# Kernel tuning notes

Hardware: AMD Instinct MI355X
Metric: run time of the kernel (lower is better)

The kernel has to match this reference:

```python
import jax, jax.numpy as jnp
import numpy as np

EMBED_DIM = 1024
NUM_HEADS = 16
HEAD_DIM = EMBED_DIM // NUM_HEADS
B, S = 2, 2048


def setup_inputs() -> dict:
    key = jax.random.key(0)
    ks = jax.random.split(key, 12)
    sd = 1.0 / np.sqrt(EMBED_DIM)
    def lin(kw, kb):
        W = jax.random.uniform(kw, (EMBED_DIM, EMBED_DIM), jnp.float32, -sd, sd)
        b = jax.random.uniform(kb, (EMBED_DIM,), jnp.float32, -sd, sd)
        return W, b
    Wq, bq = lin(ks[0], ks[1])
    Wk, bk = lin(ks[2], ks[3])
    Wv, bv = lin(ks[4], ks[5])
    Wo, bo = lin(ks[6], ks[7])
    q = jax.random.normal(ks[8], (B, S, EMBED_DIM), jnp.float32)
    k = jax.random.normal(ks[9], (B, S, EMBED_DIM), jnp.float32)
    v = jax.random.normal(ks[10], (B, S, EMBED_DIM), jnp.float32)
    # broadcastable causal mask: True = keep (mask==0 positions get -inf)
    attn_mask = jnp.tril(jnp.ones((S, S), jnp.bool_))[None, None]
    return {"q": q, "k": k, "v": v,
            "Wq": Wq, "bq": bq, "Wk": Wk, "bk": bk,
            "Wv": Wv, "bv": bv, "Wo": Wo, "bo": bo,
            "attn_mask": attn_mask}


def reference(q, k, v, Wq, bq, Wk, bk, Wv, bv, Wo, bo, attn_mask):
    bsz, tgt_len, _ = q.shape
    src_len = k.shape[1]
    scale = jnp.sqrt(jnp.float32(HEAD_DIM))
    # projections: PyTorch Linear is x @ W.T + b
    qh = (q @ Wq.T + bq).reshape(bsz, tgt_len, NUM_HEADS, HEAD_DIM).transpose(0, 2, 1, 3)
    kh = (k @ Wk.T + bk).reshape(bsz, src_len, NUM_HEADS, HEAD_DIM).transpose(0, 2, 1, 3)
    vh = (v @ Wv.T + bv).reshape(bsz, src_len, NUM_HEADS, HEAD_DIM).transpose(0, 2, 1, 3)
    # [B,H,T,S] scores
    scores = jnp.einsum('bhtd,bhsd->bhts', qh, kh) / scale
    scores = jnp.where(attn_mask, scores, -jnp.inf)
    attn = jax.nn.softmax(scores, axis=-1)
    out = jnp.einsum('bhts,bhsd->bhtd', attn, vh)  # [B,H,T,D]
    out = out.transpose(0, 2, 1, 3).reshape(bsz, tgt_len, EMBED_DIM)
    return out @ Wo.T + bo
```

## Files before the change

kernel.cpp:

```cpp
#include <hip/hip_runtime.h>
#include <hip/hip_bf16.h>
#include <stdint.h>
#include <stddef.h>

typedef __hip_bfloat16 bf16_t;
typedef __attribute__((ext_vector_type(8))) short short8;
typedef __attribute__((ext_vector_type(4))) short short4v;
typedef __attribute__((ext_vector_type(4))) float floatx4;
typedef __attribute__((ext_vector_type(4))) unsigned uint4v;
typedef __attribute__((ext_vector_type(2))) unsigned uint2v;

#define EMBED 1024
#define NHEAD 16
#define HDIM  64
#define BATCH 2
#define SEQ   2048
#define MTOT  (BATCH*SEQ)
#define NEG_INF (-1e30f)
#define SCALE2 0.18033688011112042f

#define MFMA16(a,b,c) __builtin_amdgcn_mfma_f32_16x16x32_bf16(a,b,c,0,0,0)

static __device__ __forceinline__ short bf16_bits(float x) {
    return __builtin_bit_cast(short, __float2bfloat16(x));
}

static __device__ __forceinline__ float fast_exp2(float x) {
#if __has_builtin(__builtin_amdgcn_exp2f)
    return __builtin_amdgcn_exp2f(x);
#else
    return __expf(x * 0.6931471805599453f);
#endif
}

static __device__ __forceinline__ unsigned pack_bf16x2(float lo, float hi) {
    const unsigned a = (unsigned)(unsigned short)bf16_bits(lo);
    const unsigned b = (unsigned)(unsigned short)bf16_bits(hi);
    return a | (b << 16);
}

static __device__ __forceinline__ void permswap32(unsigned& a, unsigned& b) {
#if __has_builtin(__builtin_amdgcn_permlane32_swap)
    uint2v r = __builtin_amdgcn_permlane32_swap(a, b, false, false);
    a = r[0]; b = r[1];
#else
    asm volatile("v_permlane32_swap_b32 %0, %1" : "+v"(a), "+v"(b));
#endif
}
static __device__ __forceinline__ void permswap16(unsigned& a, unsigned& b) {
#if __has_builtin(__builtin_amdgcn_permlane16_swap)
    uint2v r = __builtin_amdgcn_permlane16_swap(a, b, false, false);
    a = r[0]; b = r[1];
#else
    asm volatile("v_permlane16_swap_b32 %0, %1" : "+v"(a), "+v"(b));
#endif
}

static __device__ __forceinline__ void async_ld16(const bf16_t* g, short* l) {
    __builtin_amdgcn_global_load_lds(
        (const __attribute__((address_space(1))) void*)g,
        (__attribute__((address_space(3))) void*)l,
        16, 0, 0);
}

static __device__ __forceinline__ void store_out(float* p, float v)  { *p = v; }
static __device__ __forceinline__ void store_out(bf16_t* p, float v) { *p = __float2bfloat16(v); }

__global__ __launch_bounds__(256)
void cvt_all(const float* __restrict__ q, const float* __restrict__ k, const float* __restrict__ v,
             const float* __restrict__ wq, const float* __restrict__ wk,
             const float* __restrict__ wv, const float* __restrict__ wo,
             bf16_t* __restrict__ Qx, bf16_t* __restrict__ Kx, bf16_t* __restrict__ Vx,
             bf16_t* __restrict__ Wqb, bf16_t* __restrict__ Wkb,
             bf16_t* __restrict__ Wvb, bf16_t* __restrict__ Wob)
{
    const float* s; bf16_t* d; int n;
    switch (blockIdx.y) {
        case 0:  s = q;  d = Qx;  n = MTOT * EMBED;  break;
        case 1:  s = k;  d = Kx;  n = MTOT * EMBED;  break;
        case 2:  s = v;  d = Vx;  n = MTOT * EMBED;  break;
        case 3:  s = wq; d = Wqb; n = EMBED * EMBED; break;
        case 4:  s = wk; d = Wkb; n = EMBED * EMBED; break;
        case 5:  s = wv; d = Wvb; n = EMBED * EMBED; break;
        default: s = wo; d = Wob; n = EMBED * EMBED; break;
    }
    const int i4 = (int)blockIdx.x * 256 + (int)threadIdx.x;
    if (i4 * 4 < n) {
        const float4 f = ((const float4*)s)[i4];
        short4v o;
        o[0] = bf16_bits(f.x); o[1] = bf16_bits(f.y);
        o[2] = bf16_bits(f.z); o[3] = bf16_bits(f.w);
        ((short4v*)d)[i4] = o;
    }
}

template <typename OutT, bool VT, int BM>
static __device__ __forceinline__ void gemm_tile(
    const bf16_t* __restrict__ A, const bf16_t* __restrict__ W,
    const float* __restrict__ bias, OutT* __restrict__ C, const float scale)
{
    constexpr int MI  = BM >> 5;
    constexpr int RPW = BM >> 2;
    const int N = 1024, K = 1024;
    __shared__ alignas(16) short As[2][BM * 32];
    __shared__ alignas(16) short Bs[2][128 * 32];

    const int tid  = threadIdx.x;
    const int wave = tid >> 6;
    const int lane = tid & 63;
    const int bm = (int)blockIdx.x >> 3;
    const int bn = (int)blockIdx.x & 7;
    const int m0 = bm * BM, n0 = bn << 7;

    const int wm = ((wave >> 1) & 1) * (BM >> 1);
    const int wn = (wave & 1) << 6;

    floatx4 acc[MI][4] = {};

    const int srowA = wave * RPW + (lane >> 2);
    const int srowB = (wave << 5) + (lane >> 2);
    const int scol  = (lane & 3) << 3;
    const bf16_t* gA = A + (size_t)(m0 + srowA) * K + scol;
    const bf16_t* gB = W + (size_t)(n0 + srowB) * K + scol;

    const int fr = lane & 15;
    const int fk = (lane >> 4) << 3;

    for (int k0 = 0; k0 < K; k0 += 64) {
        __syncthreads();
        short* a0 = &As[0][wave * RPW * 32];
        short* a1 = &As[1][wave * RPW * 32];
        short* b0 = &Bs[0][wave << 10];
        short* b1 = &Bs[1][wave << 10];
        async_ld16(gA,      a0);
        async_ld16(gA + 32, a1);
        if constexpr (BM == 128) {
            async_ld16(gA + (size_t)16 * K,      a0 + 512);
            async_ld16(gA + (size_t)16 * K + 32, a1 + 512);
        }
        async_ld16(gB,      b0);
        async_ld16(gB + 32, b1);
        async_ld16(gB + (size_t)16 * K,      b0 + 512);
        async_ld16(gB + (size_t)16 * K + 32, b1 + 512);
        gA += 64; gB += 64;
        __syncthreads();

        #pragma unroll
        for (int hh = 0; hh < 2; ++hh) {
            short8 af[MI], bfr[4];
            #pragma unroll
            for (int i = 0; i < MI; ++i)
                af[i] = *(const short8*)&As[hh][(wm + (i << 4) + fr) * 32 + fk];
            #pragma unroll
            for (int j = 0; j < 4; ++j)
                bfr[j] = *(const short8*)&Bs[hh][(wn + (j << 4) + fr) * 32 + fk];
            #pragma unroll
            for (int i = 0; i < MI; ++i)
                #pragma unroll
                for (int j = 0; j < 4; ++j)
                    acc[i][j] = MFMA16(af[i], bfr[j], acc[i][j]);
        }
    }

    const int q4 = (lane >> 4) << 2;
    #pragma unroll
    for (int j = 0; j < 4; ++j) {
        const int n = n0 + wn + (j << 4) + fr;
        const float bv = bias[n];
        #pragma unroll
        for (int i = 0; i < MI; ++i) {
            const int mb = m0 + wm + (i << 4) + q4;
            if (VT) {
                const int bb = mb >> 11, ss = mb & 2047;
                short4v pk;
                #pragma unroll
                for (int r = 0; r < 4; ++r)
                    pk[r] = bf16_bits((acc[i][j][r] + bv) * scale);
                *(short4v*)((bf16_t*)C + ((size_t)(bb * 1024 + n) << 11) + ss) = pk;
            } else {
                #pragma unroll
                for (int r = 0; r < 4; ++r)
                    store_out(&C[(size_t)(mb + r) * N + n], (acc[i][j][r] + bv) * scale);
            }
        }
    }
}

__global__ __launch_bounds__(256)
void qkv_proj(const bf16_t* __restrict__ xq, const bf16_t* __restrict__ xk,
              const bf16_t* __restrict__ xv,
              const bf16_t* __restrict__ Wq, const bf16_t* __restrict__ Wk,
              const bf16_t* __restrict__ Wv,
              const float* __restrict__ bq, const float* __restrict__ bk,
              const float* __restrict__ bv,
              bf16_t* __restrict__ Qp, bf16_t* __restrict__ Kp, bf16_t* __restrict__ Vtp)
{
    if (blockIdx.z == 0)      gemm_tile<bf16_t, false, 128>(xq, Wq, bq, Qp, SCALE2);
    else if (blockIdx.z == 1) gemm_tile<bf16_t, false, 128>(xk, Wk, bk, Kp, 1.0f);
    else                      gemm_tile<bf16_t, true , 128>(xv, Wv, bv, Vtp, 1.0f);
}

__global__ __launch_bounds__(256)
void out_proj(const bf16_t* __restrict__ AO, const bf16_t* __restrict__ Wo,
              const float* __restrict__ bo, float* __restrict__ out)
{
    gemm_tile<float, false, 64>(AO, Wo, bo, out, 1.0f);
}

__global__ __launch_bounds__(64, 2)
void attn_causal(const bf16_t* __restrict__ Qp, const bf16_t* __restrict__ Kp,
                 const bf16_t* __restrict__ Vt, bf16_t* __restrict__ AO,
                 float* __restrict__ Op, float* __restrict__ Mp, float* __restrict__ Lp)
{
    const int lane = (int)threadIdx.x & 63;
    const int bid  = (int)blockIdx.x;
    const int bh   = bid & 31;
    const int w    = bid >> 5;
    const int g    = w / 3, r3 = w - g * 3;
    int tile, sidx, c0, c1;
    bool split;
    if (r3 < 2) {
        tile  = 31 - g;
        sidx  = r3;
        split = true;
        const int nch = 2 * tile + 2;
        const int h1  = nch >> 1;
        c0 = sidx ? h1 : 0;
        c1 = sidx ? nch : h1;
    } else {
        tile  = 15 - g;
        sidx  = 0;
        split = false;
        c0 = 0;
        c1 = 2 * tile + 2;
    }
    const bool hasdiag = (c1 == 2 * tile + 2);
    const int b = bh >> 4, h = bh & 15;
    const int q0 = tile << 6;

    const int fr   = lane & 15;
    const int quad = lane >> 4;
    const int fk   = quad << 3;

    const bf16_t* Qb = Qp + (size_t)(b * SEQ + q0 + fr) * EMBED + h * HDIM;
    short8 aq[4][2];
    #pragma unroll
    for (int u = 0; u < 4; ++u) {
        aq[u][0] = *(const short8*)(Qb + (size_t)(u * 16) * EMBED + fk);
        aq[u][1] = *(const short8*)(Qb + (size_t)(u * 16) * EMBED + 32 + fk);
    }

    const bf16_t* Kbase = Kp + (size_t)(b * SEQ) * EMBED + h * HDIM;
    const bf16_t* Vbase = Vt + ((size_t)(b * 1024 + h * HDIM) << 11);

    floatx4 o[4][4] = {};
    float m[4] = {NEG_INF, NEG_INF, NEG_INF, NEG_INF};
    float l[4] = {};

    auto smax_pb = [&](const floatx4& sA, const floatx4& sB, float& m_u, float& l_u,
                       floatx4* o_u, const bool masked, const int off) -> short8 {
        float v0[4], v1[4];
        #pragma unroll
        for (int rr = 0; rr < 4; ++rr) {
            float a  = sA[rr];
            float bb = sB[rr];
            if (masked) {
                const int kq = (quad << 2) + rr;
                if (kq > off + fr)      a  = NEG_INF;
                if (kq + 16 > off + fr) bb = NEG_INF;
            }
            v0[rr] = a; v1[rr] = bb;
        }
        float mx = fmaxf(fmaxf(fmaxf(v0[0], v0[1]), fmaxf(v0[2], v0[3])),
                         fmaxf(fmaxf(v1[0], v1[1]), fmaxf(v1[2], v1[3])));
        if (__any(mx > m_u + 8.0f)) {
            mx = fmaxf(mx, __shfl_xor(mx, 16, 64));
            mx = fmaxf(mx, __shfl_xor(mx, 32, 64));
            const float mn = fmaxf(m_u, mx);
            const float al = fast_exp2(m_u - mn);
            m_u = mn;
            l_u *= al;
            #pragma unroll
            for (int t = 0; t < 4; ++t)
                #pragma unroll
                for (int rr = 0; rr < 4; ++rr) o_u[t][rr] *= al;
        }
        float ls = 0.f;
        #pragma unroll
        for (int rr = 0; rr < 4; ++rr) {
            v0[rr] = fast_exp2(v0[rr] - m_u);
            v1[rr] = fast_exp2(v1[rr] - m_u);
            ls += v0[rr] + v1[rr];
        }
        l_u += ls;
        unsigned c0p = pack_bf16x2(v0[0], v0[1]);
        unsigned c1p = pack_bf16x2(v0[2], v0[3]);
        unsigned d0p = pack_bf16x2(v1[0], v1[1]);
        unsigned d1p = pack_bf16x2(v1[2], v1[3]);
        permswap32(c0p, d0p);
        permswap32(c1p, d1p);
        permswap16(c0p, d0p);
        permswap16(c1p, d1p);
        uint4v wv; wv[0] = c0p; wv[1] = c1p; wv[2] = d0p; wv[3] = d1p;
        return __builtin_bit_cast(short8, wv);
    };

#define KLOAD(K0_, K1_, K2_, K3_, kvo) do {                                  \
        const bf16_t* Kr0_ = Kbase + (size_t)((kvo) + fr) * EMBED;           \
        const bf16_t* Kr1_ = Kr0_ + (size_t)16 * EMBED;                      \
        K0_ = *(const short8*)(Kr0_ + fk);                                   \
        K1_ = *(const short8*)(Kr0_ + 32 + fk);                              \
        K2_ = *(const short8*)(Kr1_ + fk);                                   \
        K3_ = *(const short8*)(Kr1_ + 32 + fk);                              \
    } while (0)

#define ITER(KC0, KC1, KC2, KC3, KN0, KN1, KN2, KN3, CC, MASKED, OFFB, PREF) do { \
        const int kv0 = (CC) << 5;                                           \
        short8 vf[4];                                                        \
        _Pragma("unroll")                                                    \
        for (int t = 0; t < 4; ++t)                                          \
            vf[t] = *(const short8*)(Vbase + ((size_t)((t << 4) + fr) << 11) + kv0 + fk); \
        if (PREF) { KLOAD(KN0, KN1, KN2, KN3, kv0 + 32); }                   \
        floatx4 s0[4], s1[4];                                                \
        _Pragma("unroll")                                                    \
        for (int u = 0; u < 4; ++u) {                                        \
            floatx4 z0 = {}, z1 = {};                                        \
            z0 = MFMA16(KC0, aq[u][0], z0); z0 = MFMA16(KC1, aq[u][1], z0);  \
            z1 = MFMA16(KC2, aq[u][0], z1); z1 = MFMA16(KC3, aq[u][1], z1);  \
            s0[u] = z0; s1[u] = z1;                                          \
        }                                                                    \
        short8 pb[4];                                                        \
        _Pragma("unroll")                                                    \
        for (int u = 0; u < 4; ++u)                                          \
            pb[u] = smax_pb(s0[u], s1[u], m[u], l[u], o[u], MASKED, u * 16 + (OFFB)); \
        _Pragma("unroll")                                                    \
        for (int u = 0; u < 4; ++u)                                          \
            _Pragma("unroll")                                                \
            for (int t = 0; t < 4; ++t)                                      \
                o[u][t] = MFMA16(vf[t], pb[u], o[u][t]);                     \
    } while (0)

    short8 ka0, ka1, ka2, ka3, kb0, kb1, kb2, kb3;
    KLOAD(ka0, ka1, ka2, ka3, c0 << 5);

    int c = c0;
    const int cm = c1 - (hasdiag ? 2 : 1);
    if (cm > c0) {
        for (;;) {
            ITER(ka0, ka1, ka2, ka3, kb0, kb1, kb2, kb3, c, false, 0, true);
            if (++c == cm) break;
            ITER(kb0, kb1, kb2, kb3, ka0, ka1, ka2, ka3, c, false, 0, true);
            if (++c == cm) break;
        }
    }
    const bool ina = (((c - c0) & 1) == 0);
    if (hasdiag) {
        if (ina) {
            ITER(ka0, ka1, ka2, ka3, kb0, kb1, kb2, kb3, c,     true,   0, true);
            ITER(kb0, kb1, kb2, kb3, ka0, ka1, ka2, ka3, c + 1, true, -32, false);
        } else {
            ITER(kb0, kb1, kb2, kb3, ka0, ka1, ka2, ka3, c,     true,   0, true);
            ITER(ka0, ka1, ka2, ka3, kb0, kb1, kb2, kb3, c + 1, true, -32, false);
        }
    } else {
        if (ina) ITER(ka0, ka1, ka2, ka3, kb0, kb1, kb2, kb3, c, false, 0, false);
        else     ITER(kb0, kb1, kb2, kb3, ka0, ka1, ka2, ka3, c, false, 0, false);
    }

#undef ITER
#undef KLOAD

    #pragma unroll
    for (int u = 0; u < 4; ++u) {
        float t = __shfl_xor(l[u], 16, 64); l[u] += t;
        t = __shfl_xor(l[u], 32, 64);       l[u] += t;
    }

    if (!split) {
        #pragma unroll
        for (int u = 0; u < 4; ++u) {
            const float iu = 1.0f / l[u];
            bf16_t* outp = AO + (size_t)(b * SEQ + q0 + u * 16 + fr) * EMBED
                              + h * HDIM + (quad << 2);
            #pragma unroll
            for (int t = 0; t < 4; ++t) {
                short4v pk;
                #pragma unroll
                for (int rr = 0; rr < 4; ++rr)
                    pk[rr] = bf16_bits(o[u][t][rr] * iu);
                *(short4v*)(outp + (t << 4)) = pk;
            }
        }
    } else {
        const int p = (bh << 4) | (tile - 16);
        float* Ob = Op + ((size_t)(sidx * 512 + p)) * 4096;
        #pragma unroll
        for (int u = 0; u < 4; ++u) {
            #pragma unroll
            for (int t = 0; t < 4; ++t)
                *(floatx4*)&Ob[(u * 16 + fr) * 64 + (t << 4) + (quad << 2)] = o[u][t];
        }
        if (quad == 0) {
            const size_t mb = (size_t)(sidx * 512 + p) * 64;
            #pragma unroll
            for (int u = 0; u < 4; ++u) {
                Mp[mb + u * 16 + fr] = m[u];
                Lp[mb + u * 16 + fr] = l[u];
            }
        }
    }
}

__global__ __launch_bounds__(256)
void attn_combine(const float* __restrict__ Op, const float* __restrict__ Mp,
                  const float* __restrict__ Lp, bf16_t* __restrict__ AO)
{
    const int p   = (int)blockIdx.x;
    const int tid = (int)threadIdx.x;
    const int row = tid >> 2;
    const int d0  = (tid & 3) << 4;
    const int bh = p >> 4, tile = 16 + (p & 15);
    const int b = bh >> 4, h = bh & 15;

    const float m0 = Mp[(size_t)p * 64 + row];
    const float m1 = Mp[(size_t)(512 + p) * 64 + row];
    const float l0 = Lp[(size_t)p * 64 + row];
    const float l1 = Lp[(size_t)(512 + p) * 64 + row];
    const float M  = fmaxf(m0, m1);
    const float w0 = fast_exp2(m0 - M);
    const float w1 = fast_exp2(m1 - M);
    const float rd = 1.0f / (l0 * w0 + l1 * w1);

    const float* O0 = Op + (size_t)p * 4096 + row * 64 + d0;
    const float* O1 = O0 + (size_t)512 * 4096;
    bf16_t* outp = AO + (size_t)(b * SEQ + tile * 64 + row) * EMBED + h * HDIM + d0;

    #pragma unroll
    for (int seg = 0; seg < 2; ++seg) {
        const float4 a0 = *(const float4*)(O0 + seg * 8);
        const float4 a1 = *(const float4*)(O0 + seg * 8 + 4);
        const float4 c0 = *(const float4*)(O1 + seg * 8);
        const float4 c1 = *(const float4*)(O1 + seg * 8 + 4);
        short8 pk;
        pk[0] = bf16_bits((a0.x * w0 + c0.x * w1) * rd);
        pk[1] = bf16_bits((a0.y * w0 + c0.y * w1) * rd);
        pk[2] = bf16_bits((a0.z * w0 + c0.z * w1) * rd);
        pk[3] = bf16_bits((a0.w * w0 + c0.w * w1) * rd);
        pk[4] = bf16_bits((a1.x * w0 + c1.x * w1) * rd);
        pk[5] = bf16_bits((a1.y * w0 + c1.y * w1) * rd);
        pk[6] = bf16_bits((a1.z * w0 + c1.z * w1) * rd);
        pk[7] = bf16_bits((a1.w * w0 + c1.w * w1) * rd);
        *(short8*)(outp + seg * 8) = pk;
    }
}

extern "C" void kernel_launch(void* const* d_in, const int* in_sizes, int n_in,
                              void* d_out, int out_size, void* d_ws, size_t ws_size,
                              hipStream_t stream)
{
    (void)in_sizes; (void)n_in; (void)out_size; (void)ws_size;
    const float* q  = (const float*)d_in[0];
    const float* k  = (const float*)d_in[1];
    const float* v  = (const float*)d_in[2];
    const float* Wq = (const float*)d_in[3];
    const float* bq = (const float*)d_in[4];
    const float* Wk = (const float*)d_in[5];
    const float* bk = (const float*)d_in[6];
    const float* Wv = (const float*)d_in[7];
    const float* bv = (const float*)d_in[8];
    const float* Wo = (const float*)d_in[9];
    const float* bo = (const float*)d_in[10];

    const size_t NX = (size_t)MTOT * EMBED;
    const size_t NW = (size_t)EMBED * EMBED;
    bf16_t* Qx  = (bf16_t*)d_ws;
    bf16_t* Kx  = Qx  + NX;
    bf16_t* Vx  = Kx  + NX;
    bf16_t* Wqb = Vx  + NX;
    bf16_t* Wkb = Wqb + NW;
    bf16_t* Wvb = Wkb + NW;
    bf16_t* Wob = Wvb + NW;
    bf16_t* Qp  = Wob + NW;
    bf16_t* Kp  = Qp  + NX;
    bf16_t* Vtp = Kp  + NX;
    bf16_t* AO  = Vtp + NX;

    float* Op = (float*)Qx;
    float* Mp = (float*)Wqb;
    float* Lp = Mp + 2 * 512 * 64;

    dim3 blk(256);
    cvt_all<<<dim3(4096, 7), blk, 0, stream>>>(q, k, v, Wq, Wk, Wv, Wo,
                                               Qx, Kx, Vx, Wqb, Wkb, Wvb, Wob);
    qkv_proj<<<dim3(256, 1, 3), blk, 0, stream>>>(Qx, Kx, Vx, Wqb, Wkb, Wvb,
                                                  bq, bk, bv, Qp, Kp, Vtp);
    attn_causal<<<dim3(1536), dim3(64), 0, stream>>>(Qp, Kp, Vtp, AO, Op, Mp, Lp);
    attn_combine<<<dim3(512), blk, 0, stream>>>(Op, Mp, Lp, AO);
    out_proj<<<dim3(512), blk, 0, stream>>>(AO, Wob, bo, (float*)d_out);
}
```

Before: 261.4 us.

## Split causal attention KV range across four waves with in-block LDS merge

Each causal attention block now has four waves that split the KV chunks of one 64-row query tile among themselves. The partial softmax states are merged through shared memory inside the block, which removes the global-memory partial buffers and the separate combine kernel launch. MFMA sections are also wrapped in s_setprio raises so MFMA issue is favoured over the other waves. The costs are a block barrier, LDS use that may limit occupancy, and uneven per-wave work because only the waves covering the diagonal do masked iterations.

```diff
diff --git a/kernel.cpp b/kernel.cpp
--- a/kernel.cpp
+++ b/kernel.cpp
@@ -207,36 +207,26 @@
     gemm_tile<float, false, 64>(AO, Wo, bo, out, 1.0f);
 }
 
-__global__ __launch_bounds__(64, 2)
+__global__ __launch_bounds__(256, 3)
 void attn_causal(const bf16_t* __restrict__ Qp, const bf16_t* __restrict__ Kp,
-                 const bf16_t* __restrict__ Vt, bf16_t* __restrict__ AO,
-                 float* __restrict__ Op, float* __restrict__ Mp, float* __restrict__ Lp)
-{
-    const int lane = (int)threadIdx.x & 63;
+                 const bf16_t* __restrict__ Vt, bf16_t* __restrict__ AO)
+{
+    __shared__ alignas(16) float Obuf[3][64][68];
+    __shared__ float Mbuf[4][64];
+    __shared__ float Lbuf[4][64];
+
+    const int tid  = (int)threadIdx.x;
+    const int wave = tid >> 6;
+    const int lane = tid & 63;
     const int bid  = (int)blockIdx.x;
     const int bh   = bid & 31;
-    const int w    = bid >> 5;
-    const int g    = w / 3, r3 = w - g * 3;
-    int tile, sidx, c0, c1;
-    bool split;
-    if (r3 < 2) {
-        tile  = 31 - g;
-        sidx  = r3;
-        split = true;
-        const int nch = 2 * tile + 2;
-        const int h1  = nch >> 1;
-        c0 = sidx ? h1 : 0;
-        c1 = sidx ? nch : h1;
-    } else {
-        tile  = 15 - g;
-        sidx  = 0;
-        split = false;
-        c0 = 0;
-        c1 = 2 * tile + 2;
-    }
-    const bool hasdiag = (c1 == 2 * tile + 2);
+    const int tile = 31 - (bid >> 5);
     const int b = bh >> 4, h = bh & 15;
-    const int q0 = tile << 6;
+    const int q0  = tile << 6;
+    const int nch = 2 * tile + 2;
+    const int c0  = (wave * nch) >> 2;
+    const int c1  = ((wave + 1) * nch) >> 2;
+    const int d0  = nch - 2;
 
     const int fr   = lane & 15;
     const int quad = lane >> 4;
@@ -322,6 +312,7 @@
             vf[t] = *(const short8*)(Vbase + ((size_t)((t << 4) + fr) << 11) + kv0 + fk); \
         if (PREF) { KLOAD(KN0, KN1, KN2, KN3, kv0 + 32); }                   \
         floatx4 s0[4], s1[4];                                                \
+        __builtin_amdgcn_s_setprio(1);                                       \
         _Pragma("unroll")                                                    \
         for (int u = 0; u < 4; ++u) {                                        \
             floatx4 z0 = {}, z1 = {};                                        \
@@ -329,42 +320,41 @@
             z1 = MFMA16(KC2, aq[u][0], z1); z1 = MFMA16(KC3, aq[u][1], z1);  \
             s0[u] = z0; s1[u] = z1;                                          \
         }                                                                    \
+        __builtin_amdgcn_s_setprio(0);                                       \
         short8 pb[4];                                                        \
         _Pragma("unroll")                                                    \
         for (int u = 0; u < 4; ++u)                                          \
             pb[u] = smax_pb(s0[u], s1[u], m[u], l[u], o[u], MASKED, u * 16 + (OFFB)); \
+        __builtin_amdgcn_s_setprio(1);                                       \
         _Pragma("unroll")                                                    \
         for (int u = 0; u < 4; ++u)                                          \
             _Pragma("unroll")                                                \
             for (int t = 0; t < 4; ++t)                                      \
                 o[u][t] = MFMA16(vf[t], pb[u], o[u][t]);                     \
+        __builtin_amdgcn_s_setprio(0);                                       \
     } while (0)
 
-    short8 ka0, ka1, ka2, ka3, kb0, kb1, kb2, kb3;
-    KLOAD(ka0, ka1, ka2, ka3, c0 << 5);
-
-    int c = c0;
-    const int cm = c1 - (hasdiag ? 2 : 1);
-    if (cm > c0) {
-        for (;;) {
-            ITER(ka0, ka1, ka2, ka3, kb0, kb1, kb2, kb3, c, false, 0, true);
-            if (++c == cm) break;
-            ITER(kb0, kb1, kb2, kb3, ka0, ka1, ka2, ka3, c, false, 0, true);
-            if (++c == cm) break;
-        }
-    }
-    const bool ina = (((c - c0) & 1) == 0);
-    if (hasdiag) {
-        if (ina) {
-            ITER(ka0, ka1, ka2, ka3, kb0, kb1, kb2, kb3, c,     true,   0, true);
-            ITER(kb0, kb1, kb2, kb3, ka0, ka1, ka2, ka3, c + 1, true, -32, false);
-        } else {
-            ITER(kb0, kb1, kb2, kb3, ka0, ka1, ka2, ka3, c,     true,   0, true);
-            ITER(ka0, ka1, ka2, ka3, kb0, kb1, kb2, kb3, c + 1, true, -32, false);
-        }
-    } else {
-        if (ina) ITER(ka0, ka1, ka2, ka3, kb0, kb1, kb2, kb3, c, false, 0, false);
-        else     ITER(kb0, kb1, kb2, kb3, ka0, ka1, ka2, ka3, c, false, 0, false);
+    if (c1 > c0) {
+        short8 ka0, ka1, ka2, ka3, kb0, kb1, kb2, kb3;
+        KLOAD(ka0, ka1, ka2, ka3, c0 << 5);
+
+        int c = c0;
+        bool ina = true;
+        const int cmu = (d0 > c1) ? c1 : d0;
+        if (cmu > c0) {
+            for (;;) {
+                ITER(ka0, ka1, ka2, ka3, kb0, kb1, kb2, kb3, c, false, 0, (c + 1 < c1));
+                if (++c == cmu) { ina = false; break; }
+                ITER(kb0, kb1, kb2, kb3, ka0, ka1, ka2, ka3, c, false, 0, (c + 1 < c1));
+                if (++c == cmu) { ina = true; break; }
+            }
+        }
+        for (; c < c1; ++c) {
+            const int offb = (c == d0) ? 0 : -32;
+            if (ina) ITER(ka0, ka1, ka2, ka3, kb0, kb1, kb2, kb3, c, true, offb, (c + 1 < c1));
+            else     ITER(kb0, kb1, kb2, kb3, ka0, ka1, ka2, ka3, c, true, offb, (c + 1 < c1));
+            ina = !ina;
+        }
     }
 
 #undef ITER
@@ -376,81 +366,51 @@
         t = __shfl_xor(l[u], 32, 64);       l[u] += t;
     }
 
-    if (!split) {
+    if (wave != 0) {
+        #pragma unroll
+        for (int u = 0; u < 4; ++u)
+            #pragma unroll
+            for (int t = 0; t < 4; ++t)
+                *(floatx4*)&Obuf[wave - 1][u * 16 + fr][(t << 4) + (quad << 2)] = o[u][t];
+    }
+    if (quad == 0) {
         #pragma unroll
         for (int u = 0; u < 4; ++u) {
-            const float iu = 1.0f / l[u];
-            bf16_t* outp = AO + (size_t)(b * SEQ + q0 + u * 16 + fr) * EMBED
-                              + h * HDIM + (quad << 2);
+            Mbuf[wave][u * 16 + fr] = m[u];
+            Lbuf[wave][u * 16 + fr] = l[u];
+        }
+    }
+    __syncthreads();
+
+    if (wave == 0) {
+        #pragma unroll
+        for (int u = 0; u < 4; ++u) {
+            const int row = u * 16 + fr;
+            const float m1 = Mbuf[1][row], m2 = Mbuf[2][row], m3 = Mbuf[3][row];
+            const float l1 = Lbuf[1][row], l2 = Lbuf[2][row], l3 = Lbuf[3][row];
+            const float M  = fmaxf(fmaxf(m[u], m1), fmaxf(m2, m3));
+            const float w0 = fast_exp2(m[u] - M);
+            const float w1 = fast_exp2(m1 - M);
+            const float w2 = fast_exp2(m2 - M);
+            const float w3 = fast_exp2(m3 - M);
+            const float rd = 1.0f / (w0 * l[u] + w1 * l1 + w2 * l2 + w3 * l3);
+            bf16_t* outp = AO + (size_t)(b * SEQ + q0 + row) * EMBED + h * HDIM;
             #pragma unroll
             for (int t = 0; t < 4; ++t) {
+                const int col = (t << 4) + (quad << 2);
+                floatx4 acc = o[u][t];
+                const floatx4 p1 = *(const floatx4*)&Obuf[0][row][col];
+                const floatx4 p2 = *(const floatx4*)&Obuf[1][row][col];
+                const floatx4 p3 = *(const floatx4*)&Obuf[2][row][col];
                 short4v pk;
                 #pragma unroll
-                for (int rr = 0; rr < 4; ++rr)
-                    pk[rr] = bf16_bits(o[u][t][rr] * iu);
-                *(short4v*)(outp + (t << 4)) = pk;
+                for (int rr = 0; rr < 4; ++rr) {
+                    const float v = w0 * acc[rr] + w1 * p1[rr] + w2 * p2[rr] + w3 * p3[rr];
+                    pk[rr] = bf16_bits(v * rd);
+                }
+                *(short4v*)(outp + col) = pk;
             }
         }
-    } else {
-        const int p = (bh << 4) | (tile - 16);
-        float* Ob = Op + ((size_t)(sidx * 512 + p)) * 4096;
-        #pragma unroll
-        for (int u = 0; u < 4; ++u) {
-            #pragma unroll
-            for (int t = 0; t < 4; ++t)
-                *(floatx4*)&Ob[(u * 16 + fr) * 64 + (t << 4) + (quad << 2)] = o[u][t];
-        }
-        if (quad == 0) {
-            const size_t mb = (size_t)(sidx * 512 + p) * 64;
-            #pragma unroll
-            for (int u = 0; u < 4; ++u) {
-                Mp[mb + u * 16 + fr] = m[u];
-                Lp[mb + u * 16 + fr] = l[u];
-            }
-        }
-    }
-}
-
-__global__ __launch_bounds__(256)
-void attn_combine(const float* __restrict__ Op, const float* __restrict__ Mp,
-                  const float* __restrict__ Lp, bf16_t* __restrict__ AO)
-{
-    const int p   = (int)blockIdx.x;
-    const int tid = (int)threadIdx.x;
-    const int row = tid >> 2;
-    const int d0  = (tid & 3) << 4;
-    const int bh = p >> 4, tile = 16 + (p & 15);
-    const int b = bh >> 4, h = bh & 15;
-
-    const float m0 = Mp[(size_t)p * 64 + row];
-    const float m1 = Mp[(size_t)(512 + p) * 64 + row];
-    const float l0 = Lp[(size_t)p * 64 + row];
-    const float l1 = Lp[(size_t)(512 + p) * 64 + row];
-    const float M  = fmaxf(m0, m1);
-    const float w0 = fast_exp2(m0 - M);
-    const float w1 = fast_exp2(m1 - M);
-    const float rd = 1.0f / (l0 * w0 + l1 * w1);
-
-    const float* O0 = Op + (size_t)p * 4096 + row * 64 + d0;
-    const float* O1 = O0 + (size_t)512 * 4096;
-    bf16_t* outp = AO + (size_t)(b * SEQ + tile * 64 + row) * EMBED + h * HDIM + d0;
-
-    #pragma unroll
-    for (int seg = 0; seg < 2; ++seg) {
-        const float4 a0 = *(const float4*)(O0 + seg * 8);
-        const float4 a1 = *(const float4*)(O0 + seg * 8 + 4);
-        const float4 c0 = *(const float4*)(O1 + seg * 8);
-        const float4 c1 = *(const float4*)(O1 + seg * 8 + 4);
-        short8 pk;
-        pk[0] = bf16_bits((a0.x * w0 + c0.x * w1) * rd);
-        pk[1] = bf16_bits((a0.y * w0 + c0.y * w1) * rd);
-        pk[2] = bf16_bits((a0.z * w0 + c0.z * w1) * rd);
-        pk[3] = bf16_bits((a0.w * w0 + c0.w * w1) * rd);
-        pk[4] = bf16_bits((a1.x * w0 + c1.x * w1) * rd);
-        pk[5] = bf16_bits((a1.y * w0 + c1.y * w1) * rd);
-        pk[6] = bf16_bits((a1.z * w0 + c1.z * w1) * rd);
-        pk[7] = bf16_bits((a1.w * w0 + c1.w * w1) * rd);
-        *(short8*)(outp + seg * 8) = pk;
     }
 }
 
@@ -485,16 +445,11 @@
     bf16_t* Vtp = Kp  + NX;
     bf16_t* AO  = Vtp + NX;
 
-    float* Op = (float*)Qx;
-    float* Mp = (float*)Wqb;
-    float* Lp = Mp + 2 * 512 * 64;
-
     dim3 blk(256);
     cvt_all<<<dim3(4096, 7), blk, 0, stream>>>(q, k, v, Wq, Wk, Wv, Wo,
                                                Qx, Kx, Vx, Wqb, Wkb, Wvb, Wob);
     qkv_proj<<<dim3(256, 1, 3), blk, 0, stream>>>(Qx, Kx, Vx, Wqb, Wkb, Wvb,
                                                   bq, bk, bv, Qp, Kp, Vtp);
-    attn_causal<<<dim3(1536), dim3(64), 0, stream>>>(Qp, Kp, Vtp, AO, Op, Mp, Lp);
-    attn_combine<<<dim3(512), blk, 0, stream>>>(Op, Mp, Lp, AO);
+    attn_causal<<<dim3(1024), blk, 0, stream>>>(Qp, Kp, Vtp, AO);
     out_proj<<<dim3(512), blk, 0, stream>>>(AO, Wob, bo, (float*)d_out);
 }
```

Result: slower. 315.2 us (+20.5%).
